# Kernel tuning notes

Hardware: AMD Instinct MI355X
Metric: run time of the kernel (lower is better)

Reference implementation:

```python
import jax, jax.numpy as jnp
import numpy as np

B, N, C, H, L, K = 2, 21760, 256, 8, 4, 4
D = C // H
SHAPES = [(128, 128), (64, 64), (32, 32), (16, 16)]
P = sum(h * w for h, w in SHAPES)


def setup_inputs():
    ks = jax.random.split(jax.random.key(0), 24)
    s = 0.02
    def rn(i, shape, sc=s):
        return jax.random.normal(ks[i], shape, dtype=jnp.float32) * sc
    return {
        "q": jax.random.normal(ks[0], (B, N, C), dtype=jnp.float32),
        "k": jax.random.normal(ks[1], (B, P, C), dtype=jnp.float32),
        "v": jax.random.normal(ks[2], (B, P, C), dtype=jnp.float32),
        "reference_points": jax.random.uniform(ks[3], (B, N, L, 2), dtype=jnp.float32),
        "spatial_shapes": jnp.array(SHAPES, dtype=jnp.int32),
        "start_levels": jnp.array(np.cumsum([0] + [h * w for h, w in SHAPES[:-1]]), dtype=jnp.int32),
        "W_off": rn(4, (C, H * L * K * 2)),
        "b_off": rn(5, (H * L * K * 2,), 0.5),
        "W_attn": rn(6, (C, H * L * K)),
        "b_attn": rn(7, (H * L * K,)),
        "W_val": rn(8, (C, C)),
        "b_val": rn(9, (C,)),
        "W_out": rn(10, (C, C)),
        "b_out": rn(11, (C,)),
        "W1": rn(12, (C, 4 * C)),
        "b1": rn(13, (4 * C,)),
        "W2": rn(14, (4 * C, C)),
        "b2": rn(15, (C,)),
        "g1": jnp.ones((C,), jnp.float32),
        "be1": jnp.zeros((C,), jnp.float32),
        "g2": jnp.ones((C,), jnp.float32),
        "be2": jnp.zeros((C,), jnp.float32),
    }


def layer_norm(x, g, b):
    m = x.mean(-1, keepdims=True)
    var = ((x - m) ** 2).mean(-1, keepdims=True)
    return (x - m) * jax.lax.rsqrt(var + 1e-5) * g + b


def msda(q, v, reference_points, shapes_np, starts_np,
         W_off, b_off, W_attn, b_attn, W_val, b_val, W_out, b_out):
    # value projection -> (B, P, H, D)
    value = (v @ W_val + b_val).reshape(B, P, H, D)
    # learned per-query sampling offsets and attention weights
    off = (q @ W_off + b_off).reshape(B, N, H, L, K, 2)
    aw = jax.nn.softmax((q @ W_attn + b_attn).reshape(B, N, H, L * K), axis=-1)
    aw = aw.reshape(B, N, H, L, K)
    # offsets normalized by (W_l, H_l) per level
    norm = jnp.asarray(shapes_np[:, ::-1].copy(), dtype=q.dtype)  # (L, 2) = (W, H)
    loc = reference_points[:, :, None, :, None, :] + off / norm[None, None, None, :, None, :]
    out = jnp.zeros((B, N, H, D), q.dtype)
    for l in range(L):
        Hl, Wl = int(shapes_np[l, 0]), int(shapes_np[l, 1])
        s0 = int(starts_np[l])
        # (B*H, Hl*Wl, D) flattened spatial map for this level
        v_bh = value[:, s0:s0 + Hl * Wl].transpose(0, 2, 1, 3).reshape(B * H, Hl * Wl, D)
        # grid_sample align_corners=False unnormalization: x = loc*W - 0.5
        x = loc[:, :, :, l, :, 0] * Wl - 0.5  # (B, N, H, K)
        y = loc[:, :, :, l, :, 1] * Hl - 0.5
        x0 = jnp.floor(x); y0 = jnp.floor(y)
        wx = x - x0; wy = y - y0
        x0i = x0.astype(jnp.int32); y0i = y0.astype(jnp.int32)
        def samp(xi, yi):
            # zero-padding bilinear corner gather
            valid = (xi >= 0) & (xi < Wl) & (yi >= 0) & (yi < Hl)
            idx = jnp.clip(yi, 0, Hl - 1) * Wl + jnp.clip(xi, 0, Wl - 1)  # (B,N,H,K)
            idx_bh = idx.transpose(0, 2, 1, 3).reshape(B * H, N * K)
            g = jnp.take_along_axis(v_bh, idx_bh[:, :, None], axis=1)  # (B*H, N*K, D)
            g = g.reshape(B, H, N, K, D).transpose(0, 2, 1, 3, 4)
            return g * valid[..., None].astype(g.dtype)
        sampled = (samp(x0i, y0i) * ((1 - wx) * (1 - wy))[..., None]
                   + samp(x0i + 1, y0i) * (wx * (1 - wy))[..., None]
                   + samp(x0i, y0i + 1) * ((1 - wx) * wy)[..., None]
                   + samp(x0i + 1, y0i + 1) * (wx * wy)[..., None])
        out = out + (sampled * aw[:, :, :, l, :, None]).sum(axis=3)
    return out.reshape(B, N, C) @ W_out + b_out


def reference(q, k, v, reference_points, spatial_shapes, start_levels,
              W_off, b_off, W_attn, b_attn, W_val, b_val, W_out, b_out,
              W1, b1, W2, b2, g1, be1, g2, be2):
    shapes_np = np.asarray(spatial_shapes)
    starts_np = np.asarray(start_levels)
    attn = msda(q, v, reference_points, shapes_np, starts_np,
                W_off, b_off, W_attn, b_attn, W_val, b_val, W_out, b_out)
    mha_out = attn + q  # mmcv MSDA adds identity internally (dropout is identity at eval)
    x = layer_norm(q + mha_out, g1, be1)
    ffn = jax.nn.relu(x @ W1 + b1) @ W2 + b2
    return layer_norm(x + ffn, g2, be2)
```

## Files before the change

kernel.cpp:

```cpp
#include <hip/hip_runtime.h>
#include <hip/hip_bf16.h>
#include <math.h>

#define BB 2
#define NN 21760
#define CC 256
#define HH 8
#define PP 21760
#define MROWS (BB * NN)
#define VROWS (BB * PP)

typedef __attribute__((ext_vector_type(8))) short bf16x8;
typedef __attribute__((ext_vector_type(4))) float f32x4;

__device__ __forceinline__ unsigned short f2bf(float f) {
  unsigned u = __float_as_uint(f);
  u += 0x7fff + ((u >> 16) & 1);
  return (unsigned short)(u >> 16);
}
__device__ __forceinline__ float bf2f(unsigned short s) {
  return __uint_as_float(((unsigned)s) << 16);
}
__device__ __forceinline__ float bflo(unsigned u) { return __uint_as_float(u << 16); }
__device__ __forceinline__ float bfhi(unsigned u) { return __uint_as_float(u & 0xffff0000u); }

__global__ __launch_bounds__(256) void prep_all(
    const float* __restrict__ W_off, const float* __restrict__ W_at,
    const float* __restrict__ W_val,
    const float* __restrict__ W1, const float* __restrict__ W2,
    unsigned short* __restrict__ WoffT, unsigned short* __restrict__ WattnT,
    unsigned short* __restrict__ WvalT,
    unsigned short* __restrict__ W1T, unsigned short* __restrict__ W2T) {
  int i = blockIdx.x * 256 + threadIdx.x;
  if (i < 65536) {
    WoffT[i] = f2bf(W_off[(size_t)(i & 255) * 256 + (i >> 8)]);
  } else if (i < 98304) {
    int j = i - 65536;
    WattnT[j] = f2bf(W_at[(size_t)(j & 255) * 128 + (j >> 8)]);
  } else if (i < 163840) {
    int j = i - 98304;
    WvalT[j] = f2bf(W_val[(size_t)(j & 255) * 256 + (j >> 8)]);
  } else if (i < 425984) {
    int j = i - 163840;
    W1T[j] = f2bf(W1[(size_t)(j & 255) * 1024 + (j >> 8)]);
  } else if (i < 688128) {
    int j = i - 425984;
    W2T[j] = f2bf(W2[(size_t)(j & 1023) * 256 + (j >> 10)]);
  }
}

__global__ __launch_bounds__(256) void prep_wout(
    const float* __restrict__ W_out, unsigned short* __restrict__ WoutT) {
  int i = blockIdx.x * 256 + threadIdx.x;
  WoutT[i] = f2bf(W_out[(size_t)(i & 255) * 256 + (i >> 8)]);
}

template <int NC, int EPI, int FSRC>
__global__ __launch_bounds__(512, 4) void proj_mfma(
    const void* __restrict__ Ain, const unsigned short* __restrict__ BT,
    const float* __restrict__ bias,
    float* __restrict__ outF, unsigned short* __restrict__ outB) {
  constexpr int MTILE = (NC == 128) ? 64 : 32;
  __shared__ __align__(16) char xs[MTILE * 512];

  const int row0 = blockIdx.x * MTILE;
  const int t = threadIdx.x;
  const int w = t >> 6, lane = t & 63;
  const int c = lane & 15, kg = lane >> 4;
  const int mbase = (NC == 128) ? (w >> 2) * 32 : 0;
  const int nbase = (NC == 128) ? (w & 3) * 32 : w * 32;

  if (FSRC) {
    const float* A = (const float*)Ain;
    for (int i = t; i < MTILE * 128; i += 512) {
      int m = i >> 7;
      int np = i & 127;
      float2 xv = *(const float2*)(A + (size_t)(row0 + m) * 256 + np * 2);
      unsigned pk = (unsigned)f2bf(xv.x) | ((unsigned)f2bf(xv.y) << 16);
      int byte = (m * 512 + np * 4) ^ ((m & 7) << 4);
      *(unsigned*)(xs + byte) = pk;
    }
  } else {
    const unsigned short* A = (const unsigned short*)Ain;
    #pragma unroll
    for (int p = 0; p < MTILE / 16; ++p) {
      int i = t + p * 512;
      int m = i >> 5, c16 = i & 31;
      ushort4 v0 = *(const ushort4*)(A + (size_t)(row0 + m) * 256 + c16 * 8);
      ushort4 v1 = *(const ushort4*)(A + (size_t)(row0 + m) * 256 + c16 * 8 + 4);
      int byte = (m * 512 + c16 * 16) ^ ((m & 7) << 4);
      *(ushort4*)(xs + byte) = v0;
      *(ushort4*)(xs + byte + 8) = v1;
    }
  }
  __syncthreads();

  f32x4 acc[2][2];
  #pragma unroll
  for (int mf = 0; mf < 2; ++mf)
    #pragma unroll
    for (int nf = 0; nf < 2; ++nf) acc[mf][nf] = (f32x4){0.f, 0.f, 0.f, 0.f};
  #pragma unroll
  for (int kc = 0; kc < 8; ++kc) {
    int ab0 = ((mbase + c) * 512 + kc * 64 + kg * 16) ^ ((c & 7) << 4);
    int ab1 = ((mbase + 16 + c) * 512 + kc * 64 + kg * 16) ^ ((c & 7) << 4);
    bf16x8 a0 = *(const bf16x8*)(xs + ab0);
    bf16x8 a1 = *(const bf16x8*)(xs + ab1);
    #pragma unroll
    for (int nf = 0; nf < 2; ++nf) {
      bf16x8 b = *(const bf16x8*)(BT + (size_t)(nbase + nf * 16 + c) * 256 + kc * 32 + kg * 8);
      acc[0][nf] = __builtin_amdgcn_mfma_f32_16x16x32_bf16(a0, b, acc[0][nf], 0, 0, 0);
      acc[1][nf] = __builtin_amdgcn_mfma_f32_16x16x32_bf16(a1, b, acc[1][nf], 0, 0, 0);
    }
  }

  if (EPI == 0) {
    #pragma unroll
    for (int nf = 0; nf < 2; ++nf) {
      int n = nbase + nf * 16 + c;
      float bb = bias[n];
      #pragma unroll
      for (int mf = 0; mf < 2; ++mf)
        #pragma unroll
        for (int i = 0; i < 4; ++i) {
          int m = mbase + mf * 16 + kg * 4 + i;
          outF[(size_t)(row0 + m) * NC + n] = acc[mf][nf][i] + bb;
        }
    }
  } else if (EPI == 3) {
    #pragma unroll
    for (int nf = 0; nf < 2; ++nf) {
      int n = nbase + nf * 16 + c;
      float bb = bias[n];
      #pragma unroll
      for (int mf = 0; mf < 2; ++mf)
        #pragma unroll
        for (int i = 0; i < 4; ++i) {
          int m = mbase + mf * 16 + kg * 4 + i;
          outB[(size_t)(row0 + m) * NC + n] = f2bf(acc[mf][nf][i] + bb);
        }
    }
  } else {
    #pragma unroll
    for (int nf = 0; nf < 2; ++nf) {
      int n = nbase + nf * 16 + c;
      float bb = bias[n];
      #pragma unroll
      for (int mf = 0; mf < 2; ++mf)
        #pragma unroll
        for (int i = 0; i < 4; ++i) {
          float vv = acc[mf][nf][i] + bb;
          float mx = vv;
          mx = fmaxf(mx, __shfl_xor(mx, 1, 64));
          mx = fmaxf(mx, __shfl_xor(mx, 2, 64));
          mx = fmaxf(mx, __shfl_xor(mx, 4, 64));
          mx = fmaxf(mx, __shfl_xor(mx, 8, 64));
          float e = expf(vv - mx);
          float s = e;
          s += __shfl_xor(s, 1, 64);
          s += __shfl_xor(s, 2, 64);
          s += __shfl_xor(s, 4, 64);
          s += __shfl_xor(s, 8, 64);
          int m = mbase + mf * 16 + kg * 4 + i;
          outB[(size_t)(row0 + m) * NC + n] = f2bf(e / s);
        }
    }
  }
}

__global__ __launch_bounds__(256) void msda_sample(
    const unsigned short* __restrict__ value, const unsigned short* __restrict__ off,
    const unsigned short* __restrict__ aw, const float* __restrict__ refp,
    unsigned short* __restrict__ out) {
  __shared__ __align__(16) int4   s_idx[8 * 16 * 8];
  __shared__ __align__(16) float4 s_w[8 * 16 * 8];
  const int t = threadIdx.x;
  const int bn0 = blockIdx.x * 8;
  const int b = bn0 / NN;

  #pragma unroll
  for (int ss = 0; ss < 4; ++ss) {
    const int s = t + ss * 256;
    const int qi = s >> 7;
    const int j  = s & 127;
    const int bn = bn0 + qi;
    const int l  = (j >> 2) & 3;
    const int h  = j >> 4;
    const int i  = j & 15;
    const int szl = 128 >> l;
    const int st0l = (l == 0) ? 0 : (l == 1) ? 16384 : (l == 2) ? 20480 : 21504;

    unsigned op = *(const unsigned*)(off + (size_t)bn * 256 + j * 2);
    float ox = bflo(op);
    float oy = bfhi(op);
    float a  = bf2f(aw[(size_t)bn * 128 + j]);
    float rx = refp[(size_t)bn * 8 + l * 2 + 0];
    float ry = refp[(size_t)bn * 8 + l * 2 + 1];

    float x = rx * (float)szl + ox - 0.5f;
    float y = ry * (float)szl + oy - 0.5f;
    float x0f = floorf(x), y0f = floorf(y);
    float wx = x - x0f, wy = y - y0f;
    int x0 = (int)x0f, y0 = (int)y0f;
    int x1 = x0 + 1, y1 = y0 + 1;

    bool vx0 = (x0 >= 0) & (x0 < szl);
    bool vx1 = (x1 >= 0) & (x1 < szl);
    bool vy0 = (y0 >= 0) & (y0 < szl);
    bool vy1 = (y1 >= 0) & (y1 < szl);
    int cx0 = min(max(x0, 0), szl - 1);
    int cx1 = min(max(x1, 0), szl - 1);
    int cy0 = min(max(y0, 0), szl - 1);
    int cy1 = min(max(y1, 0), szl - 1);

    int base = st0l * 256 + h * 32;
    int4 iv;
    iv.x = base + (cy0 * szl + cx0) * 256;
    iv.y = base + (cy0 * szl + cx1) * 256;
    iv.z = base + (cy1 * szl + cx0) * 256;
    iv.w = base + (cy1 * szl + cx1) * 256;
    float4 wv;
    wv.x = (vx0 & vy0) ? a * (1.f - wx) * (1.f - wy) : 0.f;
    wv.y = (vx1 & vy0) ? a * wx * (1.f - wy) : 0.f;
    wv.z = (vx0 & vy1) ? a * (1.f - wx) * wy : 0.f;
    wv.w = (vx1 & vy1) ? a * wx * wy : 0.f;

    int slot = (qi * 16 + i) * 8 + h;
    s_idx[slot] = iv;
    s_w[slot] = wv;
  }
  __syncthreads();

  const int wv_ = t >> 6;
  const int lane = t & 63;
  const int qi = wv_ * 2 + (lane >> 5);
  const int h = (lane >> 2) & 7;
  const int d8 = lane & 3;
  const unsigned short* vcol = value + (size_t)b * PP * 256 + d8 * 8;

  float4 a0a = {0,0,0,0}, a0b = {0,0,0,0}, a1a = {0,0,0,0}, a1b = {0,0,0,0};
  float4 a2a = {0,0,0,0}, a2b = {0,0,0,0}, a3a = {0,0,0,0}, a3b = {0,0,0,0};
  #pragma unroll 4
  for (int i = 0; i < 16; ++i) {
    int slot = (qi * 16 + i) * 8 + h;
    int4 iv = s_idx[slot];
    float4 wv = s_w[slot];
    int4 u0 = *(const int4*)(vcol + iv.x);
    int4 u1 = *(const int4*)(vcol + iv.y);
    int4 u2 = *(const int4*)(vcol + iv.z);
    int4 u3 = *(const int4*)(vcol + iv.w);
    a0a.x += wv.x * bflo(u0.x); a0a.y += wv.x * bfhi(u0.x);
    a0a.z += wv.x * bflo(u0.y); a0a.w += wv.x * bfhi(u0.y);
    a0b.x += wv.x * bflo(u0.z); a0b.y += wv.x * bfhi(u0.z);
    a0b.z += wv.x * bflo(u0.w); a0b.w += wv.x * bfhi(u0.w);
    a1a.x += wv.y * bflo(u1.x); a1a.y += wv.y * bfhi(u1.x);
    a1a.z += wv.y * bflo(u1.y); a1a.w += wv.y * bfhi(u1.y);
    a1b.x += wv.y * bflo(u1.z); a1b.y += wv.y * bfhi(u1.z);
    a1b.z += wv.y * bflo(u1.w); a1b.w += wv.y * bfhi(u1.w);
    a2a.x += wv.z * bflo(u2.x); a2a.y += wv.z * bfhi(u2.x);
    a2a.z += wv.z * bflo(u2.y); a2a.w += wv.z * bfhi(u2.y);
    a2b.x += wv.z * bflo(u2.z); a2b.y += wv.z * bfhi(u2.z);
    a2b.z += wv.z * bflo(u2.w); a2b.w += wv.z * bfhi(u2.w);
    a3a.x += wv.w * bflo(u3.x); a3a.y += wv.w * bfhi(u3.x);
    a3a.z += wv.w * bflo(u3.y); a3a.w += wv.w * bfhi(u3.y);
    a3b.x += wv.w * bflo(u3.z); a3b.y += wv.w * bfhi(u3.z);
    a3b.z += wv.w * bflo(u3.w); a3b.w += wv.w * bfhi(u3.w);
  }
  float4 ra, rb;
  ra.x = (a0a.x + a1a.x) + (a2a.x + a3a.x);
  ra.y = (a0a.y + a1a.y) + (a2a.y + a3a.y);
  ra.z = (a0a.z + a1a.z) + (a2a.z + a3a.z);
  ra.w = (a0a.w + a1a.w) + (a2a.w + a3a.w);
  rb.x = (a0b.x + a1b.x) + (a2b.x + a3b.x);
  rb.y = (a0b.y + a1b.y) + (a2b.y + a3b.y);
  rb.z = (a0b.z + a1b.z) + (a2b.z + a3b.z);
  rb.w = (a0b.w + a1b.w) + (a2b.w + a3b.w);
  int4 ob;
  ob.x = (int)((unsigned)f2bf(ra.x) | ((unsigned)f2bf(ra.y) << 16));
  ob.y = (int)((unsigned)f2bf(ra.z) | ((unsigned)f2bf(ra.w) << 16));
  ob.z = (int)((unsigned)f2bf(rb.x) | ((unsigned)f2bf(rb.y) << 16));
  ob.w = (int)((unsigned)f2bf(rb.z) | ((unsigned)f2bf(rb.w) << 16));
  *(int4*)(out + (size_t)(bn0 + qi) * 256 + h * 32 + d8 * 8) = ob;
}

__global__ __launch_bounds__(256) void resid_ln(
    const float* __restrict__ A, const float* __restrict__ q,
    const float* __restrict__ g, const float* __restrict__ be,
    float* __restrict__ X) {
  const int row = blockIdx.x * 4 + (threadIdx.x >> 6);
  const int lane = threadIdx.x & 63;
  const size_t base = (size_t)row * 256 + lane * 4;
  float4 a = *(const float4*)(A + base);
  float4 qv = *(const float4*)(q + base);
  float4 v;
  v.x = a.x + 2.f * qv.x;
  v.y = a.y + 2.f * qv.y;
  v.z = a.z + 2.f * qv.z;
  v.w = a.w + 2.f * qv.w;
  float s = v.x + v.y + v.z + v.w;
  float s2 = v.x * v.x + v.y * v.y + v.z * v.z + v.w * v.w;
  #pragma unroll
  for (int o = 1; o < 64; o <<= 1) {
    s += __shfl_xor(s, o, 64);
    s2 += __shfl_xor(s2, o, 64);
  }
  float mean = s * (1.f / 256.f);
  float var = s2 * (1.f / 256.f) - mean * mean;
  float rstd = rsqrtf(var + 1e-5f);
  float4 gv = *(const float4*)(g + lane * 4);
  float4 bev = *(const float4*)(be + lane * 4);
  float4 o4;
  o4.x = (v.x - mean) * rstd * gv.x + bev.x;
  o4.y = (v.y - mean) * rstd * gv.y + bev.y;
  o4.z = (v.z - mean) * rstd * gv.z + bev.z;
  o4.w = (v.w - mean) * rstd * gv.w + bev.w;
  *(float4*)(X + base) = o4;
}

__global__ __launch_bounds__(512, 4) void ffn_mfma(
    const float* __restrict__ X, const unsigned short* __restrict__ W1T,
    const float* __restrict__ b1, const unsigned short* __restrict__ W2T,
    const float* __restrict__ b2, const float* __restrict__ g2,
    const float* __restrict__ be2, float* __restrict__ Out) {
  __shared__ __align__(16) char smem[16384 + 65536];
  char* xs = smem;
  char* hs = smem + 16384;
  float* out_s = (float*)(smem + 16384);

  const int row0 = blockIdx.x * 32;
  const int t = threadIdx.x;
  const int w = t >> 6, lane = t & 63;
  const int c = lane & 15, kg = lane >> 4;

  for (int i = t; i < 4096; i += 512) {
    int m = i >> 7;
    int np = i & 127;
    float2 xv = *(const float2*)(X + (size_t)(row0 + m) * 256 + np * 2);
    unsigned pk = (unsigned)f2bf(xv.x) | ((unsigned)f2bf(xv.y) << 16);
    int byte = (m * 512 + np * 4) ^ ((m & 7) << 4);
    *(unsigned*)(xs + byte) = pk;
  }
  __syncthreads();

  #pragma unroll
  for (int half = 0; half < 2; ++half) {
    f32x4 acc1[2][4];
    #pragma unroll
    for (int mf = 0; mf < 2; ++mf)
      #pragma unroll
      for (int nf = 0; nf < 4; ++nf) acc1[mf][nf] = (f32x4){0.f, 0.f, 0.f, 0.f};

    const unsigned short* wp1 = W1T + (size_t)(w * 128 + half * 64) * 256 + kg * 8;
    bf16x8 bcur[4];
    #pragma unroll
    for (int nf = 0; nf < 4; ++nf)
      bcur[nf] = *(const bf16x8*)(wp1 + (size_t)(nf * 16 + c) * 256);
    #pragma unroll
    for (int kc = 0; kc < 8; ++kc) {
      bf16x8 bnext[4];
      #pragma unroll
      for (int nf = 0; nf < 4; ++nf)
        bnext[nf] = (kc < 7)
            ? *(const bf16x8*)(wp1 + (size_t)(nf * 16 + c) * 256 + (kc + 1) * 32)
            : bcur[nf];
      int ab0 = (c * 512 + kc * 64 + kg * 16) ^ ((c & 7) << 4);
      int ab1 = ((16 + c) * 512 + kc * 64 + kg * 16) ^ ((c & 7) << 4);
      bf16x8 a0 = *(const bf16x8*)(xs + ab0);
      bf16x8 a1 = *(const bf16x8*)(xs + ab1);
      #pragma unroll
      for (int nf = 0; nf < 4; ++nf) {
        acc1[0][nf] = __builtin_amdgcn_mfma_f32_16x16x32_bf16(a0, bcur[nf], acc1[0][nf], 0, 0, 0);
        acc1[1][nf] = __builtin_amdgcn_mfma_f32_16x16x32_bf16(a1, bcur[nf], acc1[1][nf], 0, 0, 0);
      }
      #pragma unroll
      for (int nf = 0; nf < 4; ++nf) bcur[nf] = bnext[nf];
    }
    #pragma unroll
    for (int nf = 0; nf < 4; ++nf) {
      int n = w * 128 + half * 64 + nf * 16 + c;
      float bb = b1[n];
      #pragma unroll
      for (int mf = 0; mf < 2; ++mf) {
        #pragma unroll
        for (int i = 0; i < 4; ++i) {
          int m = mf * 16 + kg * 4 + i;
          float v = fmaxf(acc1[mf][nf][i] + bb, 0.f);
          int byte = (m * 2048 + n * 2) ^ ((m & 7) << 4);
          *(unsigned short*)(hs + byte) = f2bf(v);
        }
      }
    }
  }
  __syncthreads();

  f32x4 acc2[2][2];
  #pragma unroll
  for (int mf = 0; mf < 2; ++mf)
    #pragma unroll
    for (int nf = 0; nf < 2; ++nf) acc2[mf][nf] = (f32x4){0.f, 0.f, 0.f, 0.f};
  const unsigned short* wp2 = W2T + (size_t)(w * 32) * 1024 + kg * 8;
  bf16x8 b2cur[2];
  #pragma unroll
  for (int nf = 0; nf < 2; ++nf)
    b2cur[nf] = *(const bf16x8*)(wp2 + (size_t)(nf * 16 + c) * 1024);
  #pragma unroll
  for (int kc = 0; kc < 32; ++kc) {
    bf16x8 b2next[2];
    #pragma unroll
    for (int nf = 0; nf < 2; ++nf)
      b2next[nf] = (kc < 31)
          ? *(const bf16x8*)(wp2 + (size_t)(nf * 16 + c) * 1024 + (kc + 1) * 32)
          : b2cur[nf];
    int ab0 = (c * 2048 + kc * 64 + kg * 16) ^ ((c & 7) << 4);
    int ab1 = ((16 + c) * 2048 + kc * 64 + kg * 16) ^ ((c & 7) << 4);
    bf16x8 a0 = *(const bf16x8*)(hs + ab0);
    bf16x8 a1 = *(const bf16x8*)(hs + ab1);
    #pragma unroll
    for (int nf = 0; nf < 2; ++nf) {
      acc2[0][nf] = __builtin_amdgcn_mfma_f32_16x16x32_bf16(a0, b2cur[nf], acc2[0][nf], 0, 0, 0);
      acc2[1][nf] = __builtin_amdgcn_mfma_f32_16x16x32_bf16(a1, b2cur[nf], acc2[1][nf], 0, 0, 0);
    }
    #pragma unroll
    for (int nf = 0; nf < 2; ++nf) b2cur[nf] = b2next[nf];
  }
  __syncthreads();

  #pragma unroll
  for (int nf = 0; nf < 2; ++nf) {
    int n2 = w * 32 + nf * 16 + c;
    float bb = b2[n2];
    #pragma unroll
    for (int mf = 0; mf < 2; ++mf) {
      #pragma unroll
      for (int i = 0; i < 4; ++i) {
        int m = mf * 16 + kg * 4 + i;
        out_s[m * 260 + n2] = acc2[mf][nf][i] + bb + X[(size_t)(row0 + m) * 256 + n2];
      }
    }
  }
  __syncthreads();

  float4 gv = *(const float4*)(g2 + lane * 4);
  float4 bev = *(const float4*)(be2 + lane * 4);
  #pragma unroll
  for (int rr = 0; rr < 4; ++rr) {
    int r = w * 4 + rr;
    float4 v = *(const float4*)(out_s + r * 260 + lane * 4);
    float s = v.x + v.y + v.z + v.w;
    float s2 = v.x * v.x + v.y * v.y + v.z * v.z + v.w * v.w;
    #pragma unroll
    for (int o = 1; o < 64; o <<= 1) {
      s += __shfl_xor(s, o, 64);
      s2 += __shfl_xor(s2, o, 64);
    }
    float mean = s * (1.f / 256.f);
    float var = s2 * (1.f / 256.f) - mean * mean;
    float rstd = rsqrtf(var + 1e-5f);
    float4 o4;
    o4.x = (v.x - mean) * rstd * gv.x + bev.x;
    o4.y = (v.y - mean) * rstd * gv.y + bev.y;
    o4.z = (v.z - mean) * rstd * gv.z + bev.z;
    o4.w = (v.w - mean) * rstd * gv.w + bev.w;
    *(float4*)(Out + (size_t)(row0 + r) * 256 + lane * 4) = o4;
  }
}

extern "C" void kernel_launch(void* const* d_in, const int* in_sizes, int n_in,
                              void* d_out, int out_size, void* d_ws, size_t ws_size,
                              hipStream_t stream) {
  const float* q     = (const float*)d_in[0];
  const float* v     = (const float*)d_in[2];
  const float* refp  = (const float*)d_in[3];
  const float* W_off = (const float*)d_in[6];
  const float* b_off = (const float*)d_in[7];
  const float* W_at  = (const float*)d_in[8];
  const float* b_at  = (const float*)d_in[9];
  const float* W_val = (const float*)d_in[10];
  const float* b_val = (const float*)d_in[11];
  const float* W_out = (const float*)d_in[12];
  const float* b_out = (const float*)d_in[13];
  const float* W1    = (const float*)d_in[14];
  const float* b1    = (const float*)d_in[15];
  const float* W2    = (const float*)d_in[16];
  const float* b2    = (const float*)d_in[17];
  const float* g1    = (const float*)d_in[18];
  const float* be1   = (const float*)d_in[19];
  const float* g2    = (const float*)d_in[20];
  const float* be2   = (const float*)d_in[21];
  float* out = (float*)d_out;

  float* ws   = (float*)d_ws;
  float* valb = ws;
  unsigned short* valbB = (unsigned short*)valb;
  float* offb = valb + (size_t)VROWS * 256;
  unsigned short* offbB = (unsigned short*)offb;
  unsigned short* qb = (unsigned short*)(offb + (size_t)MROWS * 256);
  unsigned short* vb = qb + (size_t)MROWS * 256;
  unsigned short* msdaB = qb;
  unsigned short* awb = vb + (size_t)MROWS * 256;
  unsigned short* WoffT  = awb + (size_t)MROWS * 128;
  unsigned short* WattnT = WoffT + 65536;
  unsigned short* WvalT  = WattnT + 32768;
  unsigned short* W1T    = WvalT + 65536;
  unsigned short* W2T    = W1T + 262144;
  unsigned short* WoutT  = W2T + 262144;
  float* attnb = offb;
  float* xb = valb;

  prep_all<<<2688, 256, 0, stream>>>(W_off, W_at, W_val, W1, W2,
                                     WoffT, WattnT, WvalT, W1T, W2T);
  prep_wout<<<256, 256, 0, stream>>>(W_out, WoutT);
  proj_mfma<256, 3, 1><<<MROWS / 32, 512, 0, stream>>>(v, WvalT, b_val, nullptr, valbB);
  proj_mfma<256, 3, 1><<<MROWS / 32, 512, 0, stream>>>(q, WoffT, b_off, nullptr, offbB);
  proj_mfma<128, 1, 1><<<MROWS / 64, 512, 0, stream>>>(q, WattnT, b_at, nullptr, awb);
  msda_sample<<<MROWS / 8, 256, 0, stream>>>(valbB, offbB, awb, refp, msdaB);
  proj_mfma<256, 0, 0><<<MROWS / 32, 512, 0, stream>>>(msdaB, WoutT, b_out, attnb, nullptr);
  resid_ln<<<MROWS / 4, 256, 0, stream>>>(attnb, q, g1, be1, xb);
  ffn_mfma<<<MROWS / 32, 512, 0, stream>>>(xb, W1T, b1, W2T, b2, g2, be2, out);
}
```

Before: 438.3 us.

## Fuse offset and attention-weight projections into one q GEMM kernel

Merges the two projections that both read q (sampling offsets, 256 cols, and attention logits with softmax, 128 cols) into one kernel. Each of its 8 waves computes 48 output columns over a concatenated weight, relying on WattnT sitting directly after WoffT in memory. This reads q and converts it to bf16 once instead of twice and removes a launch. The W_out transpose is also folded into the main prep kernel to drop another launch. The risk is that the fused layout depends on the two weight buffers being contiguous.

```diff
diff --git a/kernel.cpp b/kernel.cpp
--- a/kernel.cpp
+++ b/kernel.cpp
@@ -26,10 +26,10 @@
 
 __global__ __launch_bounds__(256) void prep_all(
     const float* __restrict__ W_off, const float* __restrict__ W_at,
-    const float* __restrict__ W_val,
+    const float* __restrict__ W_val, const float* __restrict__ W_out,
     const float* __restrict__ W1, const float* __restrict__ W2,
     unsigned short* __restrict__ WoffT, unsigned short* __restrict__ WattnT,
-    unsigned short* __restrict__ WvalT,
+    unsigned short* __restrict__ WvalT, unsigned short* __restrict__ WoutT,
     unsigned short* __restrict__ W1T, unsigned short* __restrict__ W2T) {
   int i = blockIdx.x * 256 + threadIdx.x;
   if (i < 65536) {
@@ -40,19 +40,16 @@
   } else if (i < 163840) {
     int j = i - 98304;
     WvalT[j] = f2bf(W_val[(size_t)(j & 255) * 256 + (j >> 8)]);
-  } else if (i < 425984) {
+  } else if (i < 229376) {
     int j = i - 163840;
+    WoutT[j] = f2bf(W_out[(size_t)(j & 255) * 256 + (j >> 8)]);
+  } else if (i < 491520) {
+    int j = i - 229376;
     W1T[j] = f2bf(W1[(size_t)(j & 255) * 1024 + (j >> 8)]);
-  } else if (i < 688128) {
-    int j = i - 425984;
+  } else if (i < 753664) {
+    int j = i - 491520;
     W2T[j] = f2bf(W2[(size_t)(j & 1023) * 256 + (j >> 10)]);
   }
-}
-
-__global__ __launch_bounds__(256) void prep_wout(
-    const float* __restrict__ W_out, unsigned short* __restrict__ WoutT) {
-  int i = blockIdx.x * 256 + threadIdx.x;
-  WoutT[i] = f2bf(W_out[(size_t)(i & 255) * 256 + (i >> 8)]);
 }
 
 template <int NC, int EPI, int FSRC>
@@ -60,15 +57,14 @@
     const void* __restrict__ Ain, const unsigned short* __restrict__ BT,
     const float* __restrict__ bias,
     float* __restrict__ outF, unsigned short* __restrict__ outB) {
-  constexpr int MTILE = (NC == 128) ? 64 : 32;
+  constexpr int MTILE = 32;
   __shared__ __align__(16) char xs[MTILE * 512];
 
   const int row0 = blockIdx.x * MTILE;
   const int t = threadIdx.x;
   const int w = t >> 6, lane = t & 63;
   const int c = lane & 15, kg = lane >> 4;
-  const int mbase = (NC == 128) ? (w >> 2) * 32 : 0;
-  const int nbase = (NC == 128) ? (w & 3) * 32 : w * 32;
+  const int nbase = w * 32;
 
   if (FSRC) {
     const float* A = (const float*)Ain;
@@ -102,8 +98,8 @@
     for (int nf = 0; nf < 2; ++nf) acc[mf][nf] = (f32x4){0.f, 0.f, 0.f, 0.f};
   #pragma unroll
   for (int kc = 0; kc < 8; ++kc) {
-    int ab0 = ((mbase + c) * 512 + kc * 64 + kg * 16) ^ ((c & 7) << 4);
-    int ab1 = ((mbase + 16 + c) * 512 + kc * 64 + kg * 16) ^ ((c & 7) << 4);
+    int ab0 = (c * 512 + kc * 64 + kg * 16) ^ ((c & 7) << 4);
+    int ab1 = ((16 + c) * 512 + kc * 64 + kg * 16) ^ ((c & 7) << 4);
     bf16x8 a0 = *(const bf16x8*)(xs + ab0);
     bf16x8 a1 = *(const bf16x8*)(xs + ab1);
     #pragma unroll
@@ -123,11 +119,11 @@
       for (int mf = 0; mf < 2; ++mf)
         #pragma unroll
         for (int i = 0; i < 4; ++i) {
-          int m = mbase + mf * 16 + kg * 4 + i;
+          int m = mf * 16 + kg * 4 + i;
           outF[(size_t)(row0 + m) * NC + n] = acc[mf][nf][i] + bb;
         }
     }
-  } else if (EPI == 3) {
+  } else {
     #pragma unroll
     for (int nf = 0; nf < 2; ++nf) {
       int n = nbase + nf * 16 + c;
@@ -136,15 +132,69 @@
       for (int mf = 0; mf < 2; ++mf)
         #pragma unroll
         for (int i = 0; i < 4; ++i) {
-          int m = mbase + mf * 16 + kg * 4 + i;
+          int m = mf * 16 + kg * 4 + i;
           outB[(size_t)(row0 + m) * NC + n] = f2bf(acc[mf][nf][i] + bb);
         }
     }
-  } else {
-    #pragma unroll
-    for (int nf = 0; nf < 2; ++nf) {
-      int n = nbase + nf * 16 + c;
-      float bb = bias[n];
+  }
+}
+
+__global__ __launch_bounds__(512, 4) void proj_qfused(
+    const float* __restrict__ Q, const unsigned short* __restrict__ WqT,
+    const float* __restrict__ b_off, const float* __restrict__ b_at,
+    unsigned short* __restrict__ offB, unsigned short* __restrict__ awB) {
+  __shared__ __align__(16) char xs[32 * 512];
+
+  const int row0 = blockIdx.x * 32;
+  const int t = threadIdx.x;
+  const int w = t >> 6, lane = t & 63;
+  const int c = lane & 15, kg = lane >> 4;
+  const int nbase = w * 48;
+
+  for (int i = t; i < 4096; i += 512) {
+    int m = i >> 7;
+    int np = i & 127;
+    float2 xv = *(const float2*)(Q + (size_t)(row0 + m) * 256 + np * 2);
+    unsigned pk = (unsigned)f2bf(xv.x) | ((unsigned)f2bf(xv.y) << 16);
+    int byte = (m * 512 + np * 4) ^ ((m & 7) << 4);
+    *(unsigned*)(xs + byte) = pk;
+  }
+  __syncthreads();
+
+  f32x4 acc[2][3];
+  #pragma unroll
+  for (int mf = 0; mf < 2; ++mf)
+    #pragma unroll
+    for (int nf = 0; nf < 3; ++nf) acc[mf][nf] = (f32x4){0.f, 0.f, 0.f, 0.f};
+  #pragma unroll
+  for (int kc = 0; kc < 8; ++kc) {
+    int ab0 = (c * 512 + kc * 64 + kg * 16) ^ ((c & 7) << 4);
+    int ab1 = ((16 + c) * 512 + kc * 64 + kg * 16) ^ ((c & 7) << 4);
+    bf16x8 a0 = *(const bf16x8*)(xs + ab0);
+    bf16x8 a1 = *(const bf16x8*)(xs + ab1);
+    #pragma unroll
+    for (int nf = 0; nf < 3; ++nf) {
+      bf16x8 b = *(const bf16x8*)(WqT + (size_t)(nbase + nf * 16 + c) * 256 + kc * 32 + kg * 8);
+      acc[0][nf] = __builtin_amdgcn_mfma_f32_16x16x32_bf16(a0, b, acc[0][nf], 0, 0, 0);
+      acc[1][nf] = __builtin_amdgcn_mfma_f32_16x16x32_bf16(a1, b, acc[1][nf], 0, 0, 0);
+    }
+  }
+
+  #pragma unroll
+  for (int nf = 0; nf < 3; ++nf) {
+    int n = nbase + nf * 16 + c;
+    if (nbase + nf * 16 < 256) {
+      float bb = b_off[n];
+      #pragma unroll
+      for (int mf = 0; mf < 2; ++mf)
+        #pragma unroll
+        for (int i = 0; i < 4; ++i) {
+          int m = mf * 16 + kg * 4 + i;
+          offB[(size_t)(row0 + m) * 256 + n] = f2bf(acc[mf][nf][i] + bb);
+        }
+    } else {
+      int na = n - 256;
+      float bb = b_at[na];
       #pragma unroll
       for (int mf = 0; mf < 2; ++mf)
         #pragma unroll
@@ -161,8 +211,8 @@
           s += __shfl_xor(s, 2, 64);
           s += __shfl_xor(s, 4, 64);
           s += __shfl_xor(s, 8, 64);
-          int m = mbase + mf * 16 + kg * 4 + i;
-          outB[(size_t)(row0 + m) * NC + n] = f2bf(e / s);
+          int m = mf * 16 + kg * 4 + i;
+          awB[(size_t)(row0 + m) * 128 + na] = f2bf(e / s);
         }
     }
   }
@@ -507,12 +557,10 @@
   float* attnb = offb;
   float* xb = valb;
 
-  prep_all<<<2688, 256, 0, stream>>>(W_off, W_at, W_val, W1, W2,
-                                     WoffT, WattnT, WvalT, W1T, W2T);
-  prep_wout<<<256, 256, 0, stream>>>(W_out, WoutT);
+  prep_all<<<2944, 256, 0, stream>>>(W_off, W_at, W_val, W_out, W1, W2,
+                                     WoffT, WattnT, WvalT, WoutT, W1T, W2T);
   proj_mfma<256, 3, 1><<<MROWS / 32, 512, 0, stream>>>(v, WvalT, b_val, nullptr, valbB);
-  proj_mfma<256, 3, 1><<<MROWS / 32, 512, 0, stream>>>(q, WoffT, b_off, nullptr, offbB);
-  proj_mfma<128, 1, 1><<<MROWS / 64, 512, 0, stream>>>(q, WattnT, b_at, nullptr, awb);
+  proj_qfused<<<MROWS / 32, 512, 0, stream>>>(q, WoffT, b_off, b_at, offbB, awb);
   msda_sample<<<MROWS / 8, 256, 0, stream>>>(valbB, offbB, awb, refp, msdaB);
   proj_mfma<256, 0, 0><<<MROWS / 32, 512, 0, stream>>>(msdaB, WoutT, b_out, attnb, nullptr);
   resid_ln<<<MROWS / 4, 256, 0, stream>>>(attnb, q, g1, be1, xb);
```

New measurement: 428.7 us. 1.02x faster.
